# Kernel optimization log

Hardware: AMD Instinct MI355X
Metric: run time of the kernel (lower is better)

Reference implementation:

```python
import jax, jax.numpy as jnp
import numpy as np

D_IN, H1, H2, N_CLS, BATCH = 1024, 2048, 2048, 1000, 8192


def setup_inputs() -> dict:
    key = jax.random.key(0)
    ks = jax.random.split(key, 7)
    x = jax.random.normal(ks[0], (BATCH, D_IN), dtype=jnp.float32)
    # torch.nn.Linear default init scale ~ 1/sqrt(fan_in); weights stored [out, in]
    W1 = jax.random.normal(ks[1], (H1, D_IN), dtype=jnp.float32) / np.sqrt(D_IN).astype(np.float32)
    b1 = jax.random.normal(ks[2], (H1,), dtype=jnp.float32) * 0.01
    W2 = jax.random.normal(ks[3], (H2, H1), dtype=jnp.float32) / np.sqrt(H1).astype(np.float32)
    b2 = jax.random.normal(ks[4], (H2,), dtype=jnp.float32) * 0.01
    W3 = jax.random.normal(ks[5], (N_CLS, H2), dtype=jnp.float32) / np.sqrt(H2).astype(np.float32)
    b3 = jax.random.normal(ks[6], (N_CLS,), dtype=jnp.float32) * 0.01
    return {"x": x, "W1": W1, "b1": b1, "W2": W2, "b2": b2, "W3": W3, "b3": b3}


def reference(x, W1, b1, W2, b2, W3, b3):
    # forward_with_coactivations: classifier = [Linear, ReLU, Linear, ReLU, Linear]
    # activation points: the two ReLU layers and the final Linear.
    prev_act = (x > 0).astype(jnp.float32)  # [B, D_IN]

    z1 = x @ W1.T + b1                      # [B, H1]
    a1 = jax.nn.relu(z1)
    act1 = (z1 > 0).astype(jnp.float32)     # (relu(z)>0) == (z>0)
    # sum_s outer(prev_act[s], act1[s]) == prev_act.T @ act1
    coact0 = jnp.einsum('bi,bj->ij', prev_act, act1)  # [D_IN, H1]

    z2 = a1 @ W2.T + b2                     # [B, H2]
    a2 = jax.nn.relu(z2)
    act2 = (z2 > 0).astype(jnp.float32)
    coact1 = jnp.einsum('bi,bj->ij', act1, act2)      # [H1, H2]

    logits = a2 @ W3.T + b3                 # [B, N_CLS]
    act3 = (logits > 0).astype(jnp.float32)
    coact2 = jnp.einsum('bi,bj->ij', act2, act3)      # [H2, N_CLS]

    return logits, coact0, coact1, coact2
```

## Files before the change

kernel.cpp:

```cpp
#include <hip/hip_runtime.h>
#include <hip/hip_bf16.h>


typedef short v8s __attribute__((ext_vector_type(8)));
typedef float v4f __attribute__((ext_vector_type(4)));
typedef int v4i __attribute__((ext_vector_type(4)));

enum { MODE_RELU = 0, MODE_LOGITS = 1 };

__device__ __forceinline__ void async_cp16(const void* gsrc, void* ldst) {
  __builtin_amdgcn_global_load_lds(
      (const __attribute__((address_space(1))) void*)gsrc,
      (__attribute__((address_space(3))) void*)ldst, 16, 0, 0);
}

#define FENCE asm volatile("" ::: "memory")
#define BAR()                         \
  do {                                \
    FENCE;                            \
    __builtin_amdgcn_s_barrier();     \
    FENCE;                            \
  } while (0)
#define WAITL()                                          \
  do {                                                   \
    asm volatile("s_waitcnt lgkmcnt(0)" ::: "memory");   \
    __builtin_amdgcn_sched_barrier(0);                   \
  } while (0)
#define WAITV(n)                                           \
  do {                                                     \
    asm volatile("s_waitcnt vmcnt(" #n ")" ::: "memory");  \
    __builtin_amdgcn_sched_barrier(0);                     \
  } while (0)
#define PRIO1 __builtin_amdgcn_s_setprio(1)
#define PRIO0 __builtin_amdgcn_s_setprio(0)

__global__ __launch_bounds__(512, 2) void gemm256_relu_wt(
    const __hip_bfloat16* __restrict__ A, const __hip_bfloat16* __restrict__ B,
    const float* __restrict__ bias, __hip_bfloat16* __restrict__ Cout,
    char* __restrict__ Tout, int K, int ldc) {
  __shared__ char smem[131072];
  const int t = threadIdx.x;
  const int m0 = blockIdx.y * 256;
  const int n0 = blockIdx.x * 256;

  const int c0 = t, c1 = 512 + t;
  const int r0s = c0 >> 3, r1s = c1 >> 3;
  const int goff0 = r0s * K + ((c0 & 7) ^ (r0s & 7)) * 8;
  const int goff1 = r1s * K + ((c1 & 7) ^ (r1s & 7)) * 8;
  const int loff0 = c0 * 16, loff1 = c1 * 16;

  const __hip_bfloat16* const Abase = A + (size_t)m0 * K;
  const __hip_bfloat16* const Bbase = B + (size_t)n0 * K;
  const size_t hk = (size_t)128 * K;

  char* const pA0l = smem;
  char* const pA0h = smem + 16384;
  char* const pB0l = smem + 32768;
  char* const pB0h = smem + 49152;
  char* const pA1l = smem + 65536;
  char* const pA1h = smem + 81920;
  char* const pB1l = smem + 98304;
  char* const pB1h = smem + 114688;

  const int lane = t & 63;
  const int wave = t >> 6;
  const int wm = wave >> 2;
  const int wn = wave & 3;
  const int lrow = lane & 15;
  const int quad = lane >> 4;
  const int sl0 = ((quad ^ (lrow & 7)) * 16);
  const int sl1 = (((quad + 4) ^ (lrow & 7)) * 16);
  const int ardA = (wm * 128 + lrow) * 128;
  const int ardB = (wn * 64 + lrow) * 128;

  v4f acc[8][4] = {};
  v8s alo[4][2], ahi[4][2], blo[2][2], bhi[2][2];

#define STAGE(dst, src)                                               \
  do {                                                                \
    async_cp16((const void*)((src) + goff0), (void*)((dst) + loff0)); \
    async_cp16((const void*)((src) + goff1), (void*)((dst) + loff1)); \
  } while (0)

#define LDA_H(dst, hh, bb)                                                   \
  _Pragma("unroll") for (int mi = 0; mi < 4; mi++) {                         \
    dst[mi][0] =                                                             \
        *(const v8s*)(smem + (bb) + ardA + (hh)*8192 + mi * 2048 + sl0);     \
    dst[mi][1] =                                                             \
        *(const v8s*)(smem + (bb) + ardA + (hh)*8192 + mi * 2048 + sl1);     \
  }

#define LDB_P(dst, pp, bb)                                                    \
  _Pragma("unroll") for (int ni = 0; ni < 2; ni++) {                          \
    dst[ni][0] = *(const v8s*)(smem + (bb) + 32768 + ardB +                   \
                               ((pp)*2 + ni) * 2048 + sl0);                   \
    dst[ni][1] = *(const v8s*)(smem + (bb) + 32768 + ardB +                   \
                               ((pp)*2 + ni) * 2048 + sl1);                   \
  }

#define MMA_Q(af, bf, MB, NB)                                               \
  _Pragma("unroll") for (int mi = 0; mi < 4; mi++)                          \
      _Pragma("unroll") for (int ni = 0; ni < 2; ni++)                      \
          _Pragma("unroll") for (int ks = 0; ks < 2; ks++)                  \
              acc[(MB) + mi][(NB) + ni] =                                   \
      __builtin_amdgcn_mfma_f32_16x16x32_bf16(                              \
          af[mi][ks], bf[ni][ks], acc[(MB) + mi][(NB) + ni], 0, 0, 0);

  STAGE(pA0l, Abase);
  STAGE(pA0h, Abase + hk);
  STAGE(pB0l, Bbase);
  STAGE(pB0h, Bbase + hk);
  STAGE(pA1l, Abase + 64);
  WAITV(8);
  BAR();

  const int NI = K >> 7;
  const int NT = K >> 6;

#pragma unroll 1
  for (int i = 0; i < NI; ++i) {
    const int to = 2 * i + 1;
    const int t2 = (2 * i + 2 < NT) ? 2 * i + 2 : 0;
    const int t3 = (2 * i + 3 < NT) ? 2 * i + 3 : 0;
    const __hip_bfloat16* Ao = Abase + to * 64;
    const __hip_bfloat16* Bo = Bbase + to * 64;
    const __hip_bfloat16* A2 = Abase + t2 * 64;
    const __hip_bfloat16* B2 = Bbase + t2 * 64;
    const __hip_bfloat16* A3 = Abase + t3 * 64;
    LDA_H(alo, 0, 0);
    STAGE(pA1h, Ao + hk);
    WAITV(6);
    BAR();
    WAITL();
    if (i) { PRIO1; MMA_Q(ahi, bhi, 4, 2); PRIO0; }
    BAR();
    LDB_P(blo, 0, 0);
    STAGE(pB1l, Bo);
    WAITV(10);
    BAR();
    WAITL();
    PRIO1; MMA_Q(alo, blo, 0, 0); PRIO0;
    BAR();
    LDA_H(ahi, 1, 0);
    STAGE(pB1h, Bo + hk);
    WAITV(8);
    BAR();
    WAITL();
    PRIO1; MMA_Q(ahi, blo, 4, 0); PRIO0;
    BAR();
    LDB_P(bhi, 1, 0);
    STAGE(pA0l, A2);
    WAITV(8);
    BAR();
    WAITL();
    PRIO1; MMA_Q(alo, bhi, 0, 2); PRIO0;
    BAR();
    LDA_H(alo, 0, 65536);
    STAGE(pA0h, A2 + hk);
    WAITV(6);
    BAR();
    WAITL();
    PRIO1; MMA_Q(ahi, bhi, 4, 2); PRIO0;
    BAR();
    LDB_P(blo, 0, 65536);
    STAGE(pB0l, B2);
    WAITV(10);
    BAR();
    WAITL();
    PRIO1; MMA_Q(alo, blo, 0, 0); PRIO0;
    BAR();
    LDA_H(ahi, 1, 65536);
    STAGE(pB0h, B2 + hk);
    WAITV(8);
    BAR();
    WAITL();
    PRIO1; MMA_Q(ahi, blo, 4, 0); PRIO0;
    BAR();
    LDB_P(bhi, 1, 65536);
    STAGE(pA1l, A3);
    WAITV(8);
    BAR();
    WAITL();
    PRIO1; MMA_Q(alo, bhi, 0, 2); PRIO0;
    BAR();
  }
  PRIO1; MMA_Q(ahi, bhi, 4, 2); PRIO0;
  WAITV(0);
  BAR();
#undef STAGE
#undef LDA_H
#undef LDB_P
#undef MMA_Q

  float bv[4];
#pragma unroll
  for (int ni = 0; ni < 4; ni++) bv[ni] = bias[n0 + wn * 64 + ni * 16 + lrow];

#pragma unroll
  for (int mi = 0; mi < 8; mi++) {
    const int rowb = m0 + wm * 128 + mi * 16 + quad * 4;
#pragma unroll
    for (int ni = 0; ni < 4; ni++) {
      const int col = n0 + wn * 64 + ni * 16 + lrow;
#pragma unroll
      for (int r = 0; r < 4; r++) {
        const float v = acc[mi][ni][r] + bv[ni];
        Cout[(size_t)(rowb + r) * ldc + col] =
            __float2bfloat16(v > 0.f ? v : 0.f);
      }
    }
  }

  char* const sT = smem;
#pragma unroll
  for (int ni = 0; ni < 4; ni++) {
    const int c = wn * 64 + ni * 16 + lrow;
#pragma unroll
    for (int mi = 0; mi < 8; mi++) {
      const int rw = wm * 128 + mi * 16 + quad * 4;
      char4 bits;
      bits.x = (acc[mi][ni][0] + bv[ni] > 0.f) ? 1 : 0;
      bits.y = (acc[mi][ni][1] + bv[ni] > 0.f) ? 1 : 0;
      bits.z = (acc[mi][ni][2] + bv[ni] > 0.f) ? 1 : 0;
      bits.w = (acc[mi][ni][3] + bv[ni] > 0.f) ? 1 : 0;
      *(char4*)&sT[c * 272 + rw] = bits;
    }
  }
  __syncthreads();
  const int rw2 = t >> 1;
  const int hf = (t & 1) * 128;
  char* dst = Tout + (size_t)(n0 + rw2) * 8192 + m0 + hf;
  const char* src = sT + rw2 * 272 + hf;
#pragma unroll
  for (int j = 0; j < 8; j++)
    *(int4*)(dst + j * 16) = *(const int4*)(src + j * 16);
}

template <int MODE, int WT>
__global__ __launch_bounds__(256) void gemm_nt(
    const __hip_bfloat16* __restrict__ A, const __hip_bfloat16* __restrict__ B,
    const float* __restrict__ bias, void* __restrict__ Cout,
    char* __restrict__ Tout, int M, int N, int K, int n_store, int ldc) {
  __shared__ char smem[32768];
  __hip_bfloat16* sA = (__hip_bfloat16*)smem;
  __hip_bfloat16* sB = (__hip_bfloat16*)(smem + 16384);
  const int t = threadIdx.x;
  const int m0 = blockIdx.y * 128;
  const int n0 = blockIdx.x * 128;

  const __hip_bfloat16* aG[4];
  const __hip_bfloat16* bG[4];
  char* lA[4];
  char* lB[4];
#pragma unroll
  for (int j = 0; j < 4; j++) {
    const int c = j * 256 + t;
    const int row = c >> 3;
    const int g = (c & 7) ^ (row & 7);
    aG[j] = A + (size_t)(m0 + row) * K + g * 8;
    bG[j] = B + (size_t)(n0 + row) * K + g * 8;
    lA[j] = (char*)sA + c * 16;
    lB[j] = (char*)sB + c * 16;
  }

  const int lane = t & 63;
  const int wave = t >> 6;
  const int wm = (wave & 1) * 64;
  const int wn = (wave >> 1) * 64;
  const int lrow = lane & 15;
  const int quad = lane >> 4;

  const int g0 = quad ^ (lrow & 7);
  const __hip_bfloat16* pa0 = sA + (wm + lrow) * 64 + g0 * 8;
  const __hip_bfloat16* pa1 = sA + (wm + lrow) * 64 + (g0 ^ 4) * 8;
  const __hip_bfloat16* pb0 = sB + (wn + lrow) * 64 + g0 * 8;
  const __hip_bfloat16* pb1 = sB + (wn + lrow) * 64 + (g0 ^ 4) * 8;

  v4f acc[4][4] = {};

  for (int k0 = 0; k0 < K; k0 += 64) {
#pragma unroll
    for (int j = 0; j < 4; j++) {
      async_cp16(aG[j] + k0, lA[j]);
      async_cp16(bG[j] + k0, lB[j]);
    }
    __syncthreads();

    v8s a0[4], b0[4], a1[4], b1[4];
#pragma unroll
    for (int i = 0; i < 4; i++) {
      a0[i] = *(const v8s*)(pa0 + i * 16 * 64);
      b0[i] = *(const v8s*)(pb0 + i * 16 * 64);
    }
#pragma unroll
    for (int mi = 0; mi < 4; mi++)
#pragma unroll
      for (int ni = 0; ni < 4; ni++)
        acc[mi][ni] = __builtin_amdgcn_mfma_f32_16x16x32_bf16(
            a0[mi], b0[ni], acc[mi][ni], 0, 0, 0);
#pragma unroll
    for (int i = 0; i < 4; i++) {
      a1[i] = *(const v8s*)(pa1 + i * 16 * 64);
      b1[i] = *(const v8s*)(pb1 + i * 16 * 64);
    }
#pragma unroll
    for (int mi = 0; mi < 4; mi++)
#pragma unroll
      for (int ni = 0; ni < 4; ni++)
        acc[mi][ni] = __builtin_amdgcn_mfma_f32_16x16x32_bf16(
            a1[mi], b1[ni], acc[mi][ni], 0, 0, 0);
    __syncthreads();
  }

  float bvv[4];
#pragma unroll
  for (int ni = 0; ni < 4; ni++) {
    const int col = n0 + wn + ni * 16 + lrow;
    bvv[ni] = 0.f;
    if (MODE == MODE_RELU) bvv[ni] = bias[col];
    else if (col < n_store) bvv[ni] = bias[col];
  }

#pragma unroll
  for (int ni = 0; ni < 4; ni++) {
    const int col = n0 + wn + ni * 16 + lrow;
#pragma unroll
    for (int mi = 0; mi < 4; mi++) {
      const int rowb = m0 + wm + mi * 16 + quad * 4;
#pragma unroll
      for (int r = 0; r < 4; r++) {
        const int row = rowb + r;
        const float v = acc[mi][ni][r] + bvv[ni];
        if (MODE == MODE_RELU) {
          ((__hip_bfloat16*)Cout)[(size_t)row * ldc + col] =
              __float2bfloat16(v > 0.f ? v : 0.f);
        } else {
          if (col < n_store)
            ((float*)Cout)[(size_t)row * ldc + col] = v;
        }
      }
    }
  }

  if (WT) {
    char* sT = smem;
#pragma unroll
    for (int ni = 0; ni < 4; ni++) {
      const int c = wn + ni * 16 + lrow;
#pragma unroll
      for (int mi = 0; mi < 4; mi++) {
        const int r = wm + mi * 16 + quad * 4;
        char4 bits;
        bits.x = (acc[mi][ni][0] + bvv[ni] > 0.f) ? 1 : 0;
        bits.y = (acc[mi][ni][1] + bvv[ni] > 0.f) ? 1 : 0;
        bits.z = (acc[mi][ni][2] + bvv[ni] > 0.f) ? 1 : 0;
        bits.w = (acc[mi][ni][3] + bvv[ni] > 0.f) ? 1 : 0;
        *(char4*)&sT[c * 144 + r] = bits;
      }
    }
    __syncthreads();
    const int c2 = t >> 1;
    const int hf = (t & 1) * 64;
    char* dst = Tout + (size_t)(n0 + c2) * 8192 + m0 + hf;
    const char* src = sT + c2 * 144 + hf;
#pragma unroll
    for (int j = 0; j < 4; j++)
      *(int4*)(dst + j * 16) = *(const int4*)(src + j * 16);
  }
}

__global__ __launch_bounds__(256) void gemm_nt_i8(
    const char* __restrict__ A, const char* __restrict__ B,
    float* __restrict__ P, int M, int N, int Kc, int n_store, size_t slice) {
  __shared__ char sA[128 * 256];
  __shared__ char sB[128 * 256];
  const int t = threadIdx.x;
  const int m0 = blockIdx.y * 128;
  const int n0 = blockIdx.x * 128;
  const int kbeg = blockIdx.z * Kc;
  const int kend = kbeg + Kc;
  const size_t K = (size_t)Kc * gridDim.z;
  float* __restrict__ Pz = P + (size_t)blockIdx.z * slice;

  const char* aG[8];
  const char* bG[8];
  char* lA[8];
  char* lB[8];
#pragma unroll
  for (int j = 0; j < 8; j++) {
    const int c = j * 256 + t;
    const int row = c >> 4;
    const int g = (c & 15) ^ (row & 7);
    aG[j] = A + (size_t)(m0 + row) * K + g * 16;
    bG[j] = B + (size_t)(n0 + row) * K + g * 16;
    lA[j] = sA + c * 16;
    lB[j] = sB + c * 16;
  }

  const int lane = t & 63;
  const int wave = t >> 6;
  const int wm = (wave & 1) * 64;
  const int wn = (wave >> 1) * 64;
  const int lrow = lane & 15;
  const int quad = lane >> 4;

  const int g0 = quad ^ (lrow & 7);
  const char* pa[4];
  const char* pb[4];
#pragma unroll
  for (int ks = 0; ks < 4; ks++) {
    const int sl = (g0 ^ (ks * 4)) * 16;
    pa[ks] = sA + (wm + lrow) * 256 + sl;
    pb[ks] = sB + (wn + lrow) * 256 + sl;
  }

  v4i acc[4][4] = {};

  for (int k0 = kbeg; k0 < kend; k0 += 256) {
#pragma unroll
    for (int j = 0; j < 8; j++) {
      async_cp16(aG[j] + k0, lA[j]);
      async_cp16(bG[j] + k0, lB[j]);
    }
    __syncthreads();

#pragma unroll
    for (int ks = 0; ks < 4; ks++) {
      v4i a[4], b[4];
#pragma unroll
      for (int i = 0; i < 4; i++) {
        a[i] = *(const v4i*)(pa[ks] + i * 16 * 256);
        b[i] = *(const v4i*)(pb[ks] + i * 16 * 256);
      }
#pragma unroll
      for (int mi = 0; mi < 4; mi++)
#pragma unroll
        for (int ni = 0; ni < 4; ni++)
          acc[mi][ni] = __builtin_amdgcn_mfma_i32_16x16x64_i8(
              a[mi], b[ni], acc[mi][ni], 0, 0, 0);
    }
    __syncthreads();
  }

#pragma unroll
  for (int ni = 0; ni < 4; ni++) {
    const int col = n0 + wn + ni * 16 + lrow;
    if (col >= n_store) continue;
#pragma unroll
    for (int mi = 0; mi < 4; mi++) {
      const int rowb = m0 + wm + mi * 16 + quad * 4;
#pragma unroll
      for (int r = 0; r < 4; r++) {
        Pz[(size_t)(rowb + r) * n_store + col] = (float)acc[mi][ni][r];
      }
    }
  }
}

template <int Z>
__global__ __launch_bounds__(256) void reduce_part(
    const float* __restrict__ P, float* __restrict__ out, int n4, size_t slice) {
  const int i = blockIdx.x * 256 + threadIdx.x;
  if (i >= n4) return;
  float4 s = ((const float4*)P)[i];
#pragma unroll
  for (int z = 1; z < Z; z++) {
    const float4 v = ((const float4*)(P + (size_t)z * slice))[i];
    s.x += v.x; s.y += v.y; s.z += v.z; s.w += v.w;
  }
  ((float4*)out)[i] = s;
}

__global__ __launch_bounds__(256) void transpose_bin8f(
    const float* __restrict__ in, char* __restrict__ out,
    int R, int ldin, int Cphys) {
  __shared__ char tile[64][65];
  const int c0 = blockIdx.x * 64;
  const int r0 = blockIdx.y * 64;
  const int tx = threadIdx.x & 63;
  const int ty = threadIdx.x >> 6;
#pragma unroll
  for (int i = 0; i < 64; i += 4) {
    const int c = c0 + tx;
    const int r = r0 + ty + i;
    float v = 0.f;
    if (c < Cphys) v = in[(size_t)r * ldin + c];
    tile[ty + i][tx] = (v > 0.f) ? 1 : 0;
  }
  __syncthreads();
  const int u = threadIdx.x & 15;
  const int cg = threadIdx.x >> 4;
#pragma unroll
  for (int i = 0; i < 64; i += 16) {
    const int col = cg + i;
    char4 v;
    v.x = tile[4 * u + 0][col];
    v.y = tile[4 * u + 1][col];
    v.z = tile[4 * u + 2][col];
    v.w = tile[4 * u + 3][col];
    *(char4*)&out[(size_t)(c0 + col) * R + r0 + 4 * u] = v;
  }
}

struct Cvt4 {
  const float* src[4];
  __hip_bfloat16* dst[4];
  int n4[4];
};
__global__ __launch_bounds__(256) void f32_to_bf16_multi(Cvt4 c) {
  int i = blockIdx.x * 256 + threadIdx.x;
#pragma unroll
  for (int s = 0; s < 4; s++) {
    if (i < c.n4[s]) {
      const float4 v = ((const float4*)c.src[s])[i];
      union { __hip_bfloat16 h[4]; ushort4 u; } cv;
      cv.h[0] = __float2bfloat16(v.x);
      cv.h[1] = __float2bfloat16(v.y);
      cv.h[2] = __float2bfloat16(v.z);
      cv.h[3] = __float2bfloat16(v.w);
      ((ushort4*)c.dst[s])[i] = cv.u;
      return;
    }
    i -= c.n4[s];
  }
}

extern "C" void kernel_launch(void* const* d_in, const int* in_sizes, int n_in,
                              void* d_out, int out_size, void* d_ws, size_t ws_size,
                              hipStream_t stream) {
  const float* x  = (const float*)d_in[0];
  const float* W1 = (const float*)d_in[1];
  const float* b1 = (const float*)d_in[2];
  const float* W2 = (const float*)d_in[3];
  const float* b2 = (const float*)d_in[4];
  const float* W3 = (const float*)d_in[5];
  const float* b3 = (const float*)d_in[6];

  float* logits = (float*)d_out;
  float* coact0 = logits + (size_t)8192 * 1000;
  float* coact1 = coact0 + (size_t)1024 * 2048;
  float* coact2 = coact1 + (size_t)2048 * 2048;

  char* ws = (char*)d_ws;
  size_t off = 0;
  auto alloc = [&](size_t bytes) {
    char* p = ws + off;
    off += (bytes + 255) & ~(size_t)255;
    return p;
  };
  __hip_bfloat16* X   = (__hip_bfloat16*)alloc((size_t)8192 * 1024 * 2);
  __hip_bfloat16* W1b = (__hip_bfloat16*)alloc((size_t)2048 * 1024 * 2);
  __hip_bfloat16* W2b = (__hip_bfloat16*)alloc((size_t)2048 * 2048 * 2);
  __hip_bfloat16* W3b = (__hip_bfloat16*)alloc((size_t)1024 * 2048 * 2);
  __hip_bfloat16* A1  = (__hip_bfloat16*)alloc((size_t)8192 * 2048 * 2);
  __hip_bfloat16* A2  = (__hip_bfloat16*)alloc((size_t)8192 * 2048 * 2);
  char* T0 = (char*)alloc((size_t)1024 * 8192);
  char* T1 = (char*)alloc((size_t)2048 * 8192);
  char* T2 = (char*)X;
  char* T3 = (char*)W2b;
  float* P = (float*)A1;

  const dim3 blk(256);

  {
    Cvt4 c;
    c.src[0] = x;  c.dst[0] = X;   c.n4[0] = 8192 * 1024 / 4;
    c.src[1] = W1; c.dst[1] = W1b; c.n4[1] = 2048 * 1024 / 4;
    c.src[2] = W2; c.dst[2] = W2b; c.n4[2] = 2048 * 2048 / 4;
    c.src[3] = W3; c.dst[3] = W3b; c.n4[3] = 1000 * 2048 / 4;
    const int total = c.n4[0] + c.n4[1] + c.n4[2] + c.n4[3];
    f32_to_bf16_multi<<<(total + 255) / 256, blk, 0, stream>>>(c);
  }

  transpose_bin8f<<<dim3(16, 128), blk, 0, stream>>>(x, T0, 8192, 1024, 1024);

  gemm256_relu_wt<<<dim3(8, 32), dim3(512), 0, stream>>>(
      X, W1b, b1, A1, T1, 1024, 2048);

  gemm256_relu_wt<<<dim3(8, 32), dim3(512), 0, stream>>>(
      A1, W2b, b2, A2, T2, 2048, 2048);

  gemm_nt<MODE_LOGITS, 1><<<dim3(8, 64), blk, 0, stream>>>(
      A2, W3b, b3, logits, T3, 8192, 1024, 2048, 1000, 1000);

  gemm_nt_i8<<<dim3(16, 8, 4), blk, 0, stream>>>(T0, T1, P,
                                                 1024, 2048, 2048, 2048,
                                                 (size_t)1024 * 2048);
  reduce_part<4><<<1024 * 2048 / 4 / 256, blk, 0, stream>>>(
      P, coact0, 1024 * 2048 / 4, (size_t)1024 * 2048);

  gemm_nt_i8<<<dim3(16, 16, 2), blk, 0, stream>>>(T1, T2, P,
                                                  2048, 2048, 4096, 2048,
                                                  (size_t)2048 * 2048);
  reduce_part<2><<<2048 * 2048 / 4 / 256, blk, 0, stream>>>(
      P, coact1, 2048 * 2048 / 4, (size_t)2048 * 2048);

  gemm_nt_i8<<<dim3(8, 16, 4), blk, 0, stream>>>(T2, T3, P,
                                                 2048, 1024, 2048, 1000,
                                                 (size_t)2048 * 1000);
  reduce_part<4><<<2048 * 1000 / 4 / 256, blk, 0, stream>>>(
      P, coact2, 2048 * 1000 / 4, (size_t)2048 * 1000);
}
```

Baseline: 413.9 us.

## Replace int8 coactivation GEMM with 256x256 pipelined double-buffered kernel

Adds a 512-thread int8 MFMA GEMM with 256x256 tiles and the same staged async-copy, double-buffered LDS pipeline used by the bf16 ReLU GEMM, and uses it for all three coactivation products with different split-K factors. The goal is more data reuse per tile and overlap of global loads with MFMA work, replacing the old 128x128 kernel that synchronised on every k-step. It also tightens the vmcnt wait counts in the bf16 pipeline. In exchange, more split-K slices mean larger partial buffers and more reduction traffic, and the kernel uses 128KB of LDS per block.

```diff
diff --git a/kernel.cpp b/kernel.cpp
--- a/kernel.cpp
+++ b/kernel.cpp
@@ -111,7 +111,7 @@
   STAGE(pB0l, Bbase);
   STAGE(pB0h, Bbase + hk);
   STAGE(pA1l, Abase + 64);
-  WAITV(8);
+  WAITV(6);
   BAR();
 
   const int NI = K >> 7;
@@ -129,7 +129,7 @@
     const __hip_bfloat16* A3 = Abase + t3 * 64;
     LDA_H(alo, 0, 0);
     STAGE(pA1h, Ao + hk);
-    WAITV(6);
+    WAITV(4);
     BAR();
     WAITL();
     if (i) { PRIO1; MMA_Q(ahi, bhi, 4, 2); PRIO0; }
@@ -150,14 +150,14 @@
     BAR();
     LDB_P(bhi, 1, 0);
     STAGE(pA0l, A2);
-    WAITV(8);
+    WAITV(6);
     BAR();
     WAITL();
     PRIO1; MMA_Q(alo, bhi, 0, 2); PRIO0;
     BAR();
     LDA_H(alo, 0, 65536);
     STAGE(pA0h, A2 + hk);
-    WAITV(6);
+    WAITV(4);
     BAR();
     WAITL();
     PRIO1; MMA_Q(ahi, bhi, 4, 2); PRIO0;
@@ -178,7 +178,7 @@
     BAR();
     LDB_P(bhi, 1, 65536);
     STAGE(pA1l, A3);
-    WAITV(8);
+    WAITV(6);
     BAR();
     WAITL();
     PRIO1; MMA_Q(alo, bhi, 0, 2); PRIO0;
@@ -234,6 +234,180 @@
 #pragma unroll
   for (int j = 0; j < 8; j++)
     *(int4*)(dst + j * 16) = *(const int4*)(src + j * 16);
+}
+
+__global__ __launch_bounds__(512, 2) void gemm256_i8(
+    const char* __restrict__ A, const char* __restrict__ B,
+    float* __restrict__ P, int Kf, int Kc, int n_store, size_t slice) {
+  __shared__ char smem[131072];
+  const int t = threadIdx.x;
+  const int m0 = blockIdx.y * 256;
+  const int n0 = blockIdx.x * 256;
+  const int kbeg = blockIdx.z * Kc;
+  float* __restrict__ Pz = P + (size_t)blockIdx.z * slice;
+
+  const int c0 = t, c1 = 512 + t;
+  const int r0s = c0 >> 3, r1s = c1 >> 3;
+  const int goff0 = r0s * Kf + ((c0 & 7) ^ (r0s & 7)) * 16;
+  const int goff1 = r1s * Kf + ((c1 & 7) ^ (r1s & 7)) * 16;
+  const int loff0 = c0 * 16, loff1 = c1 * 16;
+
+  const char* const Abase = A + (size_t)m0 * Kf + kbeg;
+  const char* const Bbase = B + (size_t)n0 * Kf + kbeg;
+  const size_t hk = (size_t)128 * Kf;
+
+  char* const pA0l = smem;
+  char* const pA0h = smem + 16384;
+  char* const pB0l = smem + 32768;
+  char* const pB0h = smem + 49152;
+  char* const pA1l = smem + 65536;
+  char* const pA1h = smem + 81920;
+  char* const pB1l = smem + 98304;
+  char* const pB1h = smem + 114688;
+
+  const int lane = t & 63;
+  const int wave = t >> 6;
+  const int wm = wave >> 2;
+  const int wn = wave & 3;
+  const int lrow = lane & 15;
+  const int quad = lane >> 4;
+  const int sl0 = ((quad ^ (lrow & 7)) * 16);
+  const int sl1 = (((quad + 4) ^ (lrow & 7)) * 16);
+  const int ardA = (wm * 128 + lrow) * 128;
+  const int ardB = (wn * 64 + lrow) * 128;
+
+  v4i acc[8][4] = {};
+  v4i alo[4][2], ahi[4][2], blo[2][2], bhi[2][2];
+
+#define STAGE(dst, src)                                               \
+  do {                                                                \
+    async_cp16((const void*)((src) + goff0), (void*)((dst) + loff0)); \
+    async_cp16((const void*)((src) + goff1), (void*)((dst) + loff1)); \
+  } while (0)
+
+#define LDA_H(dst, hh, bb)                                                   \
+  _Pragma("unroll") for (int mi = 0; mi < 4; mi++) {                         \
+    dst[mi][0] =                                                             \
+        *(const v4i*)(smem + (bb) + ardA + (hh)*8192 + mi * 2048 + sl0);     \
+    dst[mi][1] =                                                             \
+        *(const v4i*)(smem + (bb) + ardA + (hh)*8192 + mi * 2048 + sl1);     \
+  }
+
+#define LDB_P(dst, pp, bb)                                                    \
+  _Pragma("unroll") for (int ni = 0; ni < 2; ni++) {                          \
+    dst[ni][0] = *(const v4i*)(smem + (bb) + 32768 + ardB +                   \
+                               ((pp)*2 + ni) * 2048 + sl0);                   \
+    dst[ni][1] = *(const v4i*)(smem + (bb) + 32768 + ardB +                   \
+                               ((pp)*2 + ni) * 2048 + sl1);                   \
+  }
+
+#define MMA_Q(af, bf, MB, NB)                                               \
+  _Pragma("unroll") for (int mi = 0; mi < 4; mi++)                          \
+      _Pragma("unroll") for (int ni = 0; ni < 2; ni++)                      \
+          _Pragma("unroll") for (int ks = 0; ks < 2; ks++)                  \
+              acc[(MB) + mi][(NB) + ni] =                                   \
+      __builtin_amdgcn_mfma_i32_16x16x64_i8(                                \
+          af[mi][ks], bf[ni][ks], acc[(MB) + mi][(NB) + ni], 0, 0, 0);
+
+  STAGE(pA0l, Abase);
+  STAGE(pA0h, Abase + hk);
+  STAGE(pB0l, Bbase);
+  STAGE(pB0h, Bbase + hk);
+  STAGE(pA1l, Abase + 128);
+  WAITV(6);
+  BAR();
+
+  const int NI = Kc >> 8;
+  const int NT = Kc >> 7;
+
+#pragma unroll 1
+  for (int i = 0; i < NI; ++i) {
+    const int to = 2 * i + 1;
+    const int t2 = (2 * i + 2 < NT) ? 2 * i + 2 : 0;
+    const int t3 = (2 * i + 3 < NT) ? 2 * i + 3 : 0;
+    const char* Ao = Abase + to * 128;
+    const char* Bo = Bbase + to * 128;
+    const char* A2 = Abase + t2 * 128;
+    const char* B2 = Bbase + t2 * 128;
+    const char* A3 = Abase + t3 * 128;
+    LDA_H(alo, 0, 0);
+    STAGE(pA1h, Ao + hk);
+    WAITV(4);
+    BAR();
+    WAITL();
+    if (i) { PRIO1; MMA_Q(ahi, bhi, 4, 2); PRIO0; }
+    BAR();
+    LDB_P(blo, 0, 0);
+    STAGE(pB1l, Bo);
+    WAITV(10);
+    BAR();
+    WAITL();
+    PRIO1; MMA_Q(alo, blo, 0, 0); PRIO0;
+    BAR();
+    LDA_H(ahi, 1, 0);
+    STAGE(pB1h, Bo + hk);
+    WAITV(8);
+    BAR();
+    WAITL();
+    PRIO1; MMA_Q(ahi, blo, 4, 0); PRIO0;
+    BAR();
+    LDB_P(bhi, 1, 0);
+    STAGE(pA0l, A2);
+    WAITV(6);
+    BAR();
+    WAITL();
+    PRIO1; MMA_Q(alo, bhi, 0, 2); PRIO0;
+    BAR();
+    LDA_H(alo, 0, 65536);
+    STAGE(pA0h, A2 + hk);
+    WAITV(4);
+    BAR();
+    WAITL();
+    PRIO1; MMA_Q(ahi, bhi, 4, 2); PRIO0;
+    BAR();
+    LDB_P(blo, 0, 65536);
+    STAGE(pB0l, B2);
+    WAITV(10);
+    BAR();
+    WAITL();
+    PRIO1; MMA_Q(alo, blo, 0, 0); PRIO0;
+    BAR();
+    LDA_H(ahi, 1, 65536);
+    STAGE(pB0h, B2 + hk);
+    WAITV(8);
+    BAR();
+    WAITL();
+    PRIO1; MMA_Q(ahi, blo, 4, 0); PRIO0;
+    BAR();
+    LDB_P(bhi, 1, 65536);
+    STAGE(pA1l, A3);
+    WAITV(6);
+    BAR();
+    WAITL();
+    PRIO1; MMA_Q(alo, bhi, 0, 2); PRIO0;
+    BAR();
+  }
+  PRIO1; MMA_Q(ahi, bhi, 4, 2); PRIO0;
+  WAITV(0);
+  BAR();
+#undef STAGE
+#undef LDA_H
+#undef LDB_P
+#undef MMA_Q
+
+#pragma unroll
+  for (int ni = 0; ni < 4; ni++) {
+    const int col = n0 + wn * 64 + ni * 16 + lrow;
+    if (col >= n_store) continue;
+#pragma unroll
+    for (int mi = 0; mi < 8; mi++) {
+      const int rowb = m0 + wm * 128 + mi * 16 + quad * 4;
+#pragma unroll
+      for (int r = 0; r < 4; r++) {
+        Pz[(size_t)(rowb + r) * n_store + col] = (float)acc[mi][ni][r];
+      }
+    }
+  }
 }
 
 template <int MODE, int WT>
@@ -366,94 +540,6 @@
 #pragma unroll
     for (int j = 0; j < 4; j++)
       *(int4*)(dst + j * 16) = *(const int4*)(src + j * 16);
-  }
-}
-
-__global__ __launch_bounds__(256) void gemm_nt_i8(
-    const char* __restrict__ A, const char* __restrict__ B,
-    float* __restrict__ P, int M, int N, int Kc, int n_store, size_t slice) {
-  __shared__ char sA[128 * 256];
-  __shared__ char sB[128 * 256];
-  const int t = threadIdx.x;
-  const int m0 = blockIdx.y * 128;
-  const int n0 = blockIdx.x * 128;
-  const int kbeg = blockIdx.z * Kc;
-  const int kend = kbeg + Kc;
-  const size_t K = (size_t)Kc * gridDim.z;
-  float* __restrict__ Pz = P + (size_t)blockIdx.z * slice;
-
-  const char* aG[8];
-  const char* bG[8];
-  char* lA[8];
-  char* lB[8];
-#pragma unroll
-  for (int j = 0; j < 8; j++) {
-    const int c = j * 256 + t;
-    const int row = c >> 4;
-    const int g = (c & 15) ^ (row & 7);
-    aG[j] = A + (size_t)(m0 + row) * K + g * 16;
-    bG[j] = B + (size_t)(n0 + row) * K + g * 16;
-    lA[j] = sA + c * 16;
-    lB[j] = sB + c * 16;
-  }
-
-  const int lane = t & 63;
-  const int wave = t >> 6;
-  const int wm = (wave & 1) * 64;
-  const int wn = (wave >> 1) * 64;
-  const int lrow = lane & 15;
-  const int quad = lane >> 4;
-
-  const int g0 = quad ^ (lrow & 7);
-  const char* pa[4];
-  const char* pb[4];
-#pragma unroll
-  for (int ks = 0; ks < 4; ks++) {
-    const int sl = (g0 ^ (ks * 4)) * 16;
-    pa[ks] = sA + (wm + lrow) * 256 + sl;
-    pb[ks] = sB + (wn + lrow) * 256 + sl;
-  }
-
-  v4i acc[4][4] = {};
-
-  for (int k0 = kbeg; k0 < kend; k0 += 256) {
-#pragma unroll
-    for (int j = 0; j < 8; j++) {
-      async_cp16(aG[j] + k0, lA[j]);
-      async_cp16(bG[j] + k0, lB[j]);
-    }
-    __syncthreads();
-
-#pragma unroll
-    for (int ks = 0; ks < 4; ks++) {
-      v4i a[4], b[4];
-#pragma unroll
-      for (int i = 0; i < 4; i++) {
-        a[i] = *(const v4i*)(pa[ks] + i * 16 * 256);
-        b[i] = *(const v4i*)(pb[ks] + i * 16 * 256);
-      }
-#pragma unroll
-      for (int mi = 0; mi < 4; mi++)
-#pragma unroll
-        for (int ni = 0; ni < 4; ni++)
-          acc[mi][ni] = __builtin_amdgcn_mfma_i32_16x16x64_i8(
-              a[mi], b[ni], acc[mi][ni], 0, 0, 0);
-    }
-    __syncthreads();
-  }
-
-#pragma unroll
-  for (int ni = 0; ni < 4; ni++) {
-    const int col = n0 + wn + ni * 16 + lrow;
-    if (col >= n_store) continue;
-#pragma unroll
-    for (int mi = 0; mi < 4; mi++) {
-      const int rowb = m0 + wm + mi * 16 + quad * 4;
-#pragma unroll
-      for (int r = 0; r < 4; r++) {
-        Pz[(size_t)(rowb + r) * n_store + col] = (float)acc[mi][ni][r];
-      }
-    }
   }
 }
 
@@ -583,21 +669,18 @@
   gemm_nt<MODE_LOGITS, 1><<<dim3(8, 64), blk, 0, stream>>>(
       A2, W3b, b3, logits, T3, 8192, 1024, 2048, 1000, 1000);
 
-  gemm_nt_i8<<<dim3(16, 8, 4), blk, 0, stream>>>(T0, T1, P,
-                                                 1024, 2048, 2048, 2048,
-                                                 (size_t)1024 * 2048);
-  reduce_part<4><<<1024 * 2048 / 4 / 256, blk, 0, stream>>>(
+  gemm256_i8<<<dim3(8, 4, 8), dim3(512), 0, stream>>>(
+      T0, T1, P, 8192, 1024, 2048, (size_t)1024 * 2048);
+  reduce_part<8><<<1024 * 2048 / 4 / 256, blk, 0, stream>>>(
       P, coact0, 1024 * 2048 / 4, (size_t)1024 * 2048);
 
-  gemm_nt_i8<<<dim3(16, 16, 2), blk, 0, stream>>>(T1, T2, P,
-                                                  2048, 2048, 4096, 2048,
-                                                  (size_t)2048 * 2048);
-  reduce_part<2><<<2048 * 2048 / 4 / 256, blk, 0, stream>>>(
+  gemm256_i8<<<dim3(8, 8, 4), dim3(512), 0, stream>>>(
+      T1, T2, P, 8192, 2048, 2048, (size_t)2048 * 2048);
+  reduce_part<4><<<2048 * 2048 / 4 / 256, blk, 0, stream>>>(
       P, coact1, 2048 * 2048 / 4, (size_t)2048 * 2048);
 
-  gemm_nt_i8<<<dim3(8, 16, 4), blk, 0, stream>>>(T2, T3, P,
-                                                 2048, 1024, 2048, 1000,
-                                                 (size_t)2048 * 1000);
-  reduce_part<4><<<2048 * 1000 / 4 / 256, blk, 0, stream>>>(
+  gemm256_i8<<<dim3(4, 8, 8), dim3(512), 0, stream>>>(
+      T2, T3, P, 8192, 1024, 1000, (size_t)2048 * 1000);
+  reduce_part<8><<<2048 * 1000 / 4 / 256, blk, 0, stream>>>(
       P, coact2, 2048 * 1000 / 4, (size_t)2048 * 1000);
 }
```

Result: slower. 429.7 us (+3.8%).
